# Performance work log

Hardware: AMD Instinct MI355X
Metric: run time of the kernel (lower is better)

Reference implementation:

```python
import jax, jax.numpy as jnp
import numpy as np

D_MODEL = 1024
NUM_HEADS = 16
HEAD_DIM = D_MODEL // NUM_HEADS


def setup_inputs() -> dict:
    key = jax.random.key(0)
    ks = jax.random.split(key, 12)
    B, S, D = 4, 2048, D_MODEL
    s = 1.0 / np.sqrt(D)
    return {
        "query": jax.random.normal(ks[0], (B, S, D), jnp.float32),
        "key": jax.random.normal(ks[1], (B, S, D), jnp.float32),
        "value": jax.random.normal(ks[2], (B, S, D), jnp.float32),
        "Wq": jax.random.normal(ks[3], (D, D), jnp.float32) * s,
        "bq": jax.random.normal(ks[4], (D,), jnp.float32) * 0.02,
        "Wk": jax.random.normal(ks[5], (D, D), jnp.float32) * s,
        "bk": jax.random.normal(ks[6], (D,), jnp.float32) * 0.02,
        "Wv": jax.random.normal(ks[7], (D, D), jnp.float32) * s,
        "bv": jax.random.normal(ks[8], (D,), jnp.float32) * 0.02,
        "Wo": jax.random.normal(ks[9], (D, D), jnp.float32) * s,
        "bo": jax.random.normal(ks[10], (D,), jnp.float32) * 0.02,
    }


def _split_heads(x):
    B, S, D = x.shape
    return x.reshape(B, S, NUM_HEADS, HEAD_DIM).transpose(0, 2, 1, 3)  # [B,H,S,hd]


def reference(query, key, value, Wq, bq, Wk, bk, Wv, bv, Wo, bo):
    q = _split_heads(query @ Wq + bq)
    k = _split_heads(key @ Wk + bk)
    v = _split_heads(value @ Wv + bv)
    # NOTE: original scales by 1/sqrt(d_model), not 1/sqrt(head_dim)
    scale = 1.0 / np.sqrt(D_MODEL).astype(np.float32)
    scores = jnp.einsum('bhqd,bhkd->bhqk', q, k) * scale  # [B,H,S,S]
    attn = jax.nn.softmax(scores, axis=-1)
    out = jnp.einsum('bhqk,bhkd->bhqd', attn, v)  # [B,H,S,hd]
    B, H, S, hd = out.shape
    out = out.transpose(0, 2, 1, 3).reshape(B, S, D_MODEL)
    out = out @ Wo + bo
    return out, attn
```

## Files before the change

kernel.cpp:

```cpp
#include <hip/hip_runtime.h>
#include <hip/hip_bf16.h>

typedef __bf16 bf16;
typedef __bf16 bf16x8 __attribute__((ext_vector_type(8)));
typedef __bf16 bf16x4 __attribute__((ext_vector_type(4)));
typedef float  f32x4  __attribute__((ext_vector_type(4)));

#define MFMA(A, B, C) __builtin_amdgcn_mfma_f32_16x16x32_bf16((A), (B), (C), 0, 0, 0)

static constexpr int BATCH = 4, S = 2048, D = 1024, NH = 16, HD = 64;
static constexpr int M = BATCH * S;
static constexpr float KL = 0.045084220027780106f;

__device__ __forceinline__ void gload16(const void* g, void* l) {
  __builtin_amdgcn_global_load_lds(
      (const __attribute__((address_space(1))) void*)g,
      (__attribute__((address_space(3))) void*)l, 16, 0, 0);
}

__device__ __forceinline__ float fexp2(float x) {
#if __has_builtin(__builtin_amdgcn_exp2f)
  return __builtin_amdgcn_exp2f(x);
#else
  return exp2f(x);
#endif
}

#define WAITV_BAR(n)                                        \
  asm volatile("s_waitcnt vmcnt(" #n ")" ::: "memory");     \
  __builtin_amdgcn_s_barrier();                             \
  __builtin_amdgcn_sched_barrier(0);

__global__ __launch_bounds__(256) void wt_convert(
    const float* __restrict__ W0, const float* __restrict__ W1,
    const float* __restrict__ W2, const float* __restrict__ W3,
    bf16* __restrict__ WtAll)
{
  const float* W = blockIdx.y == 0 ? W0 : blockIdx.y == 1 ? W1
                 : blockIdx.y == 2 ? W2 : W3;
  bf16* dst = WtAll + (size_t)blockIdx.y * (D * D);
  int k0 = (blockIdx.x >> 4) * 64, n0 = (blockIdx.x & 15) * 64;
  __shared__ __align__(16) bf16 T[64][72];
  int tid = threadIdx.x;
#pragma unroll
  for (int i = 0; i < 4; ++i) {
    int c = tid + i * 256, r = c >> 4, seg = c & 15;
    float4 v = *reinterpret_cast<const float4*>(W + (size_t)(k0 + r) * D + n0 + seg * 4);
    T[seg * 4 + 0][r] = (bf16)v.x; T[seg * 4 + 1][r] = (bf16)v.y;
    T[seg * 4 + 2][r] = (bf16)v.z; T[seg * 4 + 3][r] = (bf16)v.w;
  }
  __syncthreads();
#pragma unroll
  for (int i = 0; i < 2; ++i) {
    int c = tid + i * 256, r = c >> 3, seg = c & 7;
    *reinterpret_cast<bf16x8*>(dst + (size_t)(n0 + r) * D + k0 + seg * 8) =
        *reinterpret_cast<const bf16x8*>(&T[r][seg * 8]);
  }
}

__global__ __launch_bounds__(256) void x_convert(
    const float* __restrict__ X0, const float* __restrict__ X1,
    const float* __restrict__ X2, bf16* __restrict__ Y)
{
  int t = blockIdx.y;
  const float* X = t == 0 ? X0 : t == 1 ? X1 : X2;
  bf16* Yp = Y + (size_t)t * M * D;
  int idx = blockIdx.x * 256 + threadIdx.x;
#pragma unroll
  for (int i = 0; i < 4; ++i) {
    size_t j = (size_t)idx + (size_t)i * 524288;
    float4 v = reinterpret_cast<const float4*>(X)[j];
    bf16x4 o; o[0] = (bf16)v.x; o[1] = (bf16)v.y; o[2] = (bf16)v.z; o[3] = (bf16)v.w;
    reinterpret_cast<bf16x4*>(Yp)[j] = o;
  }
}

__global__ __launch_bounds__(256) void qkv_gemm(
    const bf16* __restrict__ Xb, const bf16* __restrict__ WtAll,
    const float* __restrict__ bq, const float* __restrict__ bk, const float* __restrict__ bv,
    bf16* __restrict__ Qb, bf16* __restrict__ Kb, bf16* __restrict__ Vtb)
{
  int v = blockIdx.y;
  const bf16*  X    = Xb + (size_t)v * M * D;
  const bf16*  Wt   = WtAll + (size_t)v * (D * D);
  const float* bias = v == 0 ? bq : v == 1 ? bk : bv;

  int x = blockIdx.x;
  int swz = (x & 7) * 64 + (x >> 3);
  int mt = swz >> 3, nt = swz & 7;
  int m0 = mt * 128, n0 = nt * 128;
  int tid = threadIdx.x, lane = tid & 63, w = tid >> 6;
  int wm = (w >> 1) * 64, wn = (w & 1) * 64;
  int lr = lane & 15, lg = lane >> 4;

  __shared__ __align__(16) unsigned char smem[34816];
  auto As = reinterpret_cast<bf16(*)[128][32]>(smem);
  auto Bs = reinterpret_cast<bf16(*)[128][32]>(smem + 16384);

  f32x4 acc[4][4] = {};

  int srow = w * 32 + (lane >> 2);
  int scol = (lane & 3) * 8;

  auto stage = [&](int buf, int ks) {
    const bf16* ga = X + (size_t)(m0 + srow) * D + ks * 32 + scol;
    bf16* la = &As[buf][w * 32][0];
    gload16(ga, la);
    gload16(ga + 16 * D, la + 16 * 32);
    const bf16* gb = Wt + (size_t)(n0 + srow) * D + ks * 32 + scol;
    bf16* lb = &Bs[buf][w * 32][0];
    gload16(gb, lb);
    gload16(gb + 16 * D, lb + 16 * 32);
  };

  stage(0, 0);
  for (int ks = 0; ks < 32; ++ks) {
    __syncthreads();
    if (ks < 31) stage((ks + 1) & 1, ks + 1);
    int buf = ks & 1;
    bf16x8 af[4], bfr[4];
#pragma unroll
    for (int i = 0; i < 4; ++i)
      af[i] = *reinterpret_cast<const bf16x8*>(&As[buf][wm + i * 16 + lr][8 * lg]);
#pragma unroll
    for (int j = 0; j < 4; ++j)
      bfr[j] = *reinterpret_cast<const bf16x8*>(&Bs[buf][wn + j * 16 + lr][8 * lg]);
#pragma unroll
    for (int i = 0; i < 4; ++i)
#pragma unroll
      for (int j = 0; j < 4; ++j)
        acc[i][j] = MFMA(af[i], bfr[j], acc[i][j]);
  }
  __syncthreads();

  if (v < 2) {
    bf16* Out = v == 0 ? Qb : Kb;
    float qs = v == 0 ? KL : 1.0f;
    auto Es = reinterpret_cast<bf16(*)[128]>(smem);
#pragma unroll
    for (int i = 0; i < 4; ++i)
#pragma unroll
      for (int j = 0; j < 4; ++j) {
        int n = wn + j * 16 + lr;
        float bias_n = bias[n0 + n];
#pragma unroll
        for (int r = 0; r < 4; ++r)
          Es[wm + i * 16 + 4 * lg + r][n] = (bf16)((acc[i][j][r] + bias_n) * qs);
      }
    __syncthreads();
#pragma unroll
    for (int i = 0; i < 8; ++i) {
      int c = tid + i * 256, r = c >> 4, seg = c & 15;
      int mg = m0 + r, b = mg >> 11, s = mg & 2047;
      int ng = n0 + seg * 8, h = ng >> 6, d = ng & 63;
      *reinterpret_cast<bf16x8*>(Out + (((size_t)(b * NH + h)) * S + s) * HD + d) =
          *reinterpret_cast<const bf16x8*>(&Es[r][seg * 8]);
    }
  } else {
    auto Es = reinterpret_cast<bf16(*)[136]>(smem);
#pragma unroll
    for (int i = 0; i < 4; ++i)
#pragma unroll
      for (int j = 0; j < 4; ++j) {
        int n = wn + j * 16 + lr;
        float bias_n = bias[n0 + n];
        bf16x4 t;
#pragma unroll
        for (int r = 0; r < 4; ++r) t[r] = (bf16)(acc[i][j][r] + bias_n);
        *reinterpret_cast<bf16x4*>(&Es[n][wm + i * 16 + 4 * lg]) = t;
      }
    __syncthreads();
#pragma unroll
    for (int i = 0; i < 8; ++i) {
      int c = tid + i * 256, r = c >> 4, seg = c & 15;
      int ng = n0 + r, h = ng >> 6, d = ng & 63;
      int mg = m0 + seg * 8, b = mg >> 11, s = mg & 2047;
      *reinterpret_cast<bf16x8*>(Vtb + (((size_t)(b * NH + h)) * HD + d) * S + s) =
          *reinterpret_cast<const bf16x8*>(&Es[r][seg * 8]);
    }
  }
}

__global__ __launch_bounds__(256) void attn_kernel(
    const bf16* __restrict__ Qb, const bf16* __restrict__ Kb, const bf16* __restrict__ Vtb,
    float* __restrict__ attn_out, bf16* __restrict__ ctx)
{
  int xx = blockIdx.x;
  int xcd = xx & 7, r8 = xx >> 3;
  int bh = xcd + 8 * (r8 >> 5);
  int qb = r8 & 31;
  int tid = threadIdx.x, lane = tid & 63, w = tid >> 6;
  int lr = lane & 15, lg = lane >> 4;
  int sw = lr & 7;

  __shared__ __align__(16) bf16 Ks[2][64][64];
  __shared__ __align__(16) bf16 Vs[2][64][64];
  __shared__ __align__(16) bf16 Ps[4][16][40];

  int q_row = qb * 64 + w * 16 + lr;
  const bf16x8* Qp = reinterpret_cast<const bf16x8*>(Qb + ((size_t)bh * S + q_row) * HD);
  bf16x8 qf0 = Qp[lg], qf1 = Qp[4 + lg];

  auto stageK = [&](int buf, int kc) {
    const bf16* base = Kb + ((size_t)bh * S + kc * 64) * HD;
#pragma unroll
    for (int i = 0; i < 2; ++i) {
      int c = i * 256 + tid, row = c >> 3, j = c & 7;
      gload16(base + row * HD + 8 * (j ^ (row & 7)),
              reinterpret_cast<bf16*>(&Ks[buf][0][0]) + c * 8);
    }
  };
  auto stageV = [&](int buf, int kc) {
    const bf16* base = Vtb + (size_t)bh * HD * S + kc * 64;
#pragma unroll
    for (int i = 0; i < 2; ++i) {
      int c = i * 256 + tid, row = c >> 3, j = c & 7;
      gload16(base + (size_t)row * S + 8 * (j ^ (row & 7)),
              reinterpret_cast<bf16*>(&Vs[buf][0][0]) + c * 8);
    }
  };

  float lrun = 0.f;
  stageK(0, 0);
  for (int kc = 0; kc < 32; ++kc) {
    if (kc < 31) {
      stageK((kc + 1) & 1, kc + 1);
      WAITV_BAR(2)
    } else {
      WAITV_BAR(0)
    }
    int buf = kc & 1;
#pragma unroll
    for (int sub = 0; sub < 4; ++sub) {
      int row = sub * 16 + lr;
      bf16x8 k0 = *reinterpret_cast<const bf16x8*>(&Ks[buf][row][8 * (lg ^ sw)]);
      bf16x8 k1 = *reinterpret_cast<const bf16x8*>(&Ks[buf][row][8 * ((lg + 4) ^ sw)]);
      f32x4 sa = {};
      sa = MFMA(k0, qf0, sa);
      sa = MFMA(k1, qf1, sa);
      lrun += fexp2(sa[0]) + fexp2(sa[1]) + fexp2(sa[2]) + fexp2(sa[3]);
    }
    __builtin_amdgcn_s_barrier();
  }
  lrun += __shfl_xor(lrun, 16);
  lrun += __shfl_xor(lrun, 32);
  float lg2l = __log2f(lrun);

  f32x4 oacc[4] = {};
  float* arow = attn_out + ((size_t)bh * S + q_row) * S;

  auto computeB = [&](int buf, int kc) {
#pragma unroll
    for (int half = 0; half < 2; ++half) {
      f32x4 sg[2];
#pragma unroll
      for (int t = 0; t < 2; ++t) {
        int row = (half * 2 + t) * 16 + lr;
        bf16x8 k0 = *reinterpret_cast<const bf16x8*>(&Ks[buf][row][8 * (lg ^ sw)]);
        bf16x8 k1 = *reinterpret_cast<const bf16x8*>(&Ks[buf][row][8 * ((lg + 4) ^ sw)]);
        f32x4 sa = {};
        sa = MFMA(k0, qf0, sa);
        sa = MFMA(k1, qf1, sa);
        sg[t] = sa;
      }
#pragma unroll
      for (int t = 0; t < 2; ++t) {
        f32x4 pv;
        bf16x4 pb;
#pragma unroll
        for (int r = 0; r < 4; ++r) {
          float p = fexp2(sg[t][r] - lg2l);
          pv[r] = p; pb[r] = (bf16)p;
        }
        __builtin_nontemporal_store(pv,
            reinterpret_cast<f32x4*>(arow + kc * 64 + half * 32 + t * 16 + 4 * lg));
        *reinterpret_cast<bf16x4*>(&Ps[w][lr][t * 16 + 4 * lg]) = pb;
      }
      bf16x8 pa = *reinterpret_cast<const bf16x8*>(&Ps[w][lr][8 * lg]);
#pragma unroll
      for (int dt = 0; dt < 4; ++dt) {
        int vrow = dt * 16 + lr;
        bf16x8 vb = *reinterpret_cast<const bf16x8*>(&Vs[buf][vrow][8 * ((half * 4 + lg) ^ sw)]);
        oacc[dt] = MFMA(pa, vb, oacc[dt]);
      }
    }
  };

  stageK(0, 0); stageV(0, 0);
  stageK(1, 1); stageV(1, 1);
  WAITV_BAR(4)
  computeB(0, 0);
  __builtin_amdgcn_s_barrier();

  for (int kc = 1; kc < 32; ++kc) {
    if (kc < 31) {
      stageK((kc + 1) & 1, kc + 1);
      stageV((kc + 1) & 1, kc + 1);
      WAITV_BAR(8)
    } else {
      WAITV_BAR(4)
    }
    computeB(kc & 1, kc);
    __builtin_amdgcn_s_barrier();
  }

  int b = bh >> 4, h = bh & 15;
  bf16* cs = reinterpret_cast<bf16*>(&Ks[0][0][0]) + w * (16 * 72);
#pragma unroll
  for (int dt = 0; dt < 4; ++dt)
#pragma unroll
    for (int r = 0; r < 4; ++r)
      cs[(4 * lg + r) * 72 + dt * 16 + lr] = (bf16)oacc[dt][r];
  asm volatile("s_waitcnt lgkmcnt(0)" ::: "memory");
  __builtin_amdgcn_sched_barrier(0);
  {
    int r_ = lane >> 2, cb = (lane & 3) * 16;
    int qr = qb * 64 + w * 16 + r_;
    bf16* cp = ctx + ((size_t)b * S + qr) * D + h * HD + cb;
    *reinterpret_cast<bf16x8*>(cp)     = *reinterpret_cast<const bf16x8*>(&cs[r_ * 72 + cb]);
    *reinterpret_cast<bf16x8*>(cp + 8) = *reinterpret_cast<const bf16x8*>(&cs[r_ * 72 + cb + 8]);
  }
}

__global__ __launch_bounds__(256) void out_gemm(
    const bf16* __restrict__ ctx, const bf16* __restrict__ Wto,
    const float* __restrict__ bo, float* __restrict__ Out)
{
  int x = blockIdx.x;
  int swz = (x & 7) * 64 + (x >> 3);
  int mt = swz >> 3, nt = swz & 7;
  int m0 = mt * 128, n0 = nt * 128;
  int tid = threadIdx.x, lane = tid & 63, w = tid >> 6;
  int wm = (w >> 1) * 64, wn = (w & 1) * 64;
  int lr = lane & 15, lg = lane >> 4;

  __shared__ __align__(16) bf16 As[2][128][32];
  __shared__ __align__(16) bf16 Bs[2][128][32];

  f32x4 acc[4][4] = {};

  int srow = w * 32 + (lane >> 2);
  int scol = (lane & 3) * 8;

  auto stage = [&](int buf, int ks) {
    const bf16* ga = ctx + (size_t)(m0 + srow) * D + ks * 32 + scol;
    bf16* la = &As[buf][w * 32][0];
    gload16(ga, la);
    gload16(ga + 16 * D, la + 16 * 32);
    const bf16* gb = Wto + (size_t)(n0 + srow) * D + ks * 32 + scol;
    bf16* lb = &Bs[buf][w * 32][0];
    gload16(gb, lb);
    gload16(gb + 16 * D, lb + 16 * 32);
  };

  stage(0, 0);
  for (int ks = 0; ks < 32; ++ks) {
    __syncthreads();
    if (ks < 31) stage((ks + 1) & 1, ks + 1);
    int buf = ks & 1;
    bf16x8 af[4], bfr[4];
#pragma unroll
    for (int i = 0; i < 4; ++i)
      af[i] = *reinterpret_cast<const bf16x8*>(&As[buf][wm + i * 16 + lr][8 * lg]);
#pragma unroll
    for (int j = 0; j < 4; ++j)
      bfr[j] = *reinterpret_cast<const bf16x8*>(&Bs[buf][wn + j * 16 + lr][8 * lg]);
#pragma unroll
    for (int i = 0; i < 4; ++i)
#pragma unroll
      for (int j = 0; j < 4; ++j)
        acc[i][j] = MFMA(af[i], bfr[j], acc[i][j]);
  }

#pragma unroll
  for (int i = 0; i < 4; ++i)
#pragma unroll
    for (int j = 0; j < 4; ++j) {
      int n = n0 + wn + j * 16 + lr;
      float bias_n = bo[n];
#pragma unroll
      for (int r = 0; r < 4; ++r)
        Out[(size_t)(m0 + wm + i * 16 + 4 * lg + r) * D + n] = acc[i][j][r] + bias_n;
    }
}

extern "C" void kernel_launch(void* const* d_in, const int* in_sizes, int n_in,
                              void* d_out, int out_size, void* d_ws, size_t ws_size,
                              hipStream_t stream)
{
  const float* query = (const float*)d_in[0];
  const float* key   = (const float*)d_in[1];
  const float* value = (const float*)d_in[2];
  const float* Wq = (const float*)d_in[3]; const float* bq = (const float*)d_in[4];
  const float* Wk = (const float*)d_in[5]; const float* bk = (const float*)d_in[6];
  const float* Wv = (const float*)d_in[7]; const float* bv = (const float*)d_in[8];
  const float* Wo = (const float*)d_in[9]; const float* bo = (const float*)d_in[10];

  float* out  = (float*)d_out;
  float* attn = out + (size_t)M * D;

  char* ws = (char*)d_ws;
  const size_t MiB = 1048576;
  bf16* WtAll = (bf16*)ws;
  bf16* Xb    = (bf16*)(ws + 8 * MiB);
  bf16* Qb    = (bf16*)(ws + 56 * MiB);
  bf16* Kb    = (bf16*)(ws + 72 * MiB);
  bf16* Vtb   = (bf16*)(ws + 88 * MiB);
  bf16* ctx   = Xb;

  wt_convert<<<dim3(256, 4), 256, 0, stream>>>(Wq, Wk, Wv, Wo, WtAll);
  x_convert<<<dim3(2048, 3), 256, 0, stream>>>(query, key, value, Xb);
  qkv_gemm<<<dim3(512, 3), 256, 0, stream>>>(Xb, WtAll, bq, bk, bv, Qb, Kb, Vtb);
  attn_kernel<<<dim3(2048), 256, 0, stream>>>(Qb, Kb, Vtb, attn, ctx);
  out_gemm<<<dim3(512), 256, 0, stream>>>(ctx, WtAll + (size_t)3 * D * D, bo, out);
}
```

Baseline: 456.1 us.

## Switch attention kernel to 32x32 MFMA with 2x2 query/key wave split

```diff
diff --git a/kernel.cpp b/kernel.cpp
--- a/kernel.cpp
+++ b/kernel.cpp
@@ -4,9 +4,13 @@
 typedef __bf16 bf16;
 typedef __bf16 bf16x8 __attribute__((ext_vector_type(8)));
 typedef __bf16 bf16x4 __attribute__((ext_vector_type(4)));
+typedef __bf16 bf16x2 __attribute__((ext_vector_type(2)));
 typedef float  f32x4  __attribute__((ext_vector_type(4)));
-
-#define MFMA(A, B, C) __builtin_amdgcn_mfma_f32_16x16x32_bf16((A), (B), (C), 0, 0, 0)
+typedef float  f32x16 __attribute__((ext_vector_type(16)));
+typedef unsigned int u32;
+
+#define MFMA(A, B, C)   __builtin_amdgcn_mfma_f32_16x16x32_bf16((A), (B), (C), 0, 0, 0)
+#define MFMA32(A, B, C) __builtin_amdgcn_mfma_f32_32x32x16_bf16((A), (B), (C), 0, 0, 0)
 
 static constexpr int BATCH = 4, S = 2048, D = 1024, NH = 16, HD = 64;
 static constexpr int M = BATCH * S;
@@ -25,6 +29,14 @@
   return exp2f(x);
 #endif
 }
+
+__device__ __forceinline__ u32 pack2(float a, float b) {
+  union { bf16x2 h; u32 u; } c;
+  c.h = (bf16x2){(bf16)a, (bf16)b};
+  return c.u;
+}
+
+union U4 { u32 w[4]; bf16x8 v; };
 
 #define WAITV_BAR(n)                                        \
   asm volatile("s_waitcnt vmcnt(" #n ")" ::: "memory");     \
@@ -190,16 +202,19 @@
   int bh = xcd + 8 * (r8 >> 5);
   int qb = r8 & 31;
   int tid = threadIdx.x, lane = tid & 63, w = tid >> 6;
-  int lr = lane & 15, lg = lane >> 4;
-  int sw = lr & 7;
+  int q32 = lane & 31, hi = lane >> 5;
+  int qh = w & 1, kh = w >> 1;
 
   __shared__ __align__(16) bf16 Ks[2][64][64];
   __shared__ __align__(16) bf16 Vs[2][64][64];
-  __shared__ __align__(16) bf16 Ps[4][16][40];
-
-  int q_row = qb * 64 + w * 16 + lr;
-  const bf16x8* Qp = reinterpret_cast<const bf16x8*>(Qb + ((size_t)bh * S + q_row) * HD);
-  bf16x8 qf0 = Qp[lg], qf1 = Qp[4 + lg];
+  __shared__ float sums[2][64];
+
+  int q_row = qb * 64 + qh * 32 + q32;
+  const bf16* Qrow = Qb + ((size_t)bh * S + q_row) * HD;
+  bf16x8 qreg[4];
+#pragma unroll
+  for (int c = 0; c < 4; ++c)
+    qreg[c] = *reinterpret_cast<const bf16x8*>(Qrow + c * 16 + 8 * hi);
 
   auto stageK = [&](int buf, int kc) {
     const bf16* base = Kb + ((size_t)bh * S + kc * 64) * HD;
@@ -219,6 +234,8 @@
               reinterpret_cast<bf16*>(&Vs[buf][0][0]) + c * 8);
     }
   };
+
+  int krow = kh * 32 + q32, ks7 = krow & 7;
 
   float lrun = 0.f;
   stageK(0, 0);
@@ -230,58 +247,66 @@
       WAITV_BAR(0)
     }
     int buf = kc & 1;
-#pragma unroll
-    for (int sub = 0; sub < 4; ++sub) {
-      int row = sub * 16 + lr;
-      bf16x8 k0 = *reinterpret_cast<const bf16x8*>(&Ks[buf][row][8 * (lg ^ sw)]);
-      bf16x8 k1 = *reinterpret_cast<const bf16x8*>(&Ks[buf][row][8 * ((lg + 4) ^ sw)]);
-      f32x4 sa = {};
-      sa = MFMA(k0, qf0, sa);
-      sa = MFMA(k1, qf1, sa);
-      lrun += fexp2(sa[0]) + fexp2(sa[1]) + fexp2(sa[2]) + fexp2(sa[3]);
-    }
+    f32x16 sa = {};
+#pragma unroll
+    for (int c = 0; c < 4; ++c) {
+      bf16x8 kf = *reinterpret_cast<const bf16x8*>(&Ks[buf][krow][8 * ((2 * c + hi) ^ ks7)]);
+      sa = MFMA32(kf, qreg[c], sa);
+    }
+#pragma unroll
+    for (int r = 0; r < 16; ++r) lrun += fexp2(sa[r]);
     __builtin_amdgcn_s_barrier();
   }
-  lrun += __shfl_xor(lrun, 16);
   lrun += __shfl_xor(lrun, 32);
-  float lg2l = __log2f(lrun);
-
-  f32x4 oacc[4] = {};
+  if (hi == 0) sums[kh][qh * 32 + q32] = lrun;
+  __syncthreads();
+  float lg2l = __log2f(sums[0][qh * 32 + q32] + sums[1][qh * 32 + q32]);
+
+  f32x16 oaccA = {}, oaccB = {};
   float* arow = attn_out + ((size_t)bh * S + q_row) * S;
 
   auto computeB = [&](int buf, int kc) {
-#pragma unroll
-    for (int half = 0; half < 2; ++half) {
-      f32x4 sg[2];
-#pragma unroll
-      for (int t = 0; t < 2; ++t) {
-        int row = (half * 2 + t) * 16 + lr;
-        bf16x8 k0 = *reinterpret_cast<const bf16x8*>(&Ks[buf][row][8 * (lg ^ sw)]);
-        bf16x8 k1 = *reinterpret_cast<const bf16x8*>(&Ks[buf][row][8 * ((lg + 4) ^ sw)]);
-        f32x4 sa = {};
-        sa = MFMA(k0, qf0, sa);
-        sa = MFMA(k1, qf1, sa);
-        sg[t] = sa;
+    f32x16 sa = {};
+#pragma unroll
+    for (int c = 0; c < 4; ++c) {
+      bf16x8 kf = *reinterpret_cast<const bf16x8*>(&Ks[buf][krow][8 * ((2 * c + hi) ^ ks7)]);
+      sa = MFMA32(kf, qreg[c], sa);
+    }
+    u32 pku[8];
+#pragma unroll
+    for (int rq = 0; rq < 4; ++rq) {
+      f32x4 pv;
+#pragma unroll
+      for (int j = 0; j < 4; ++j) pv[j] = fexp2(sa[rq * 4 + j] - lg2l);
+      __builtin_nontemporal_store(pv,
+          reinterpret_cast<f32x4*>(arow + kc * 64 + kh * 32 + 8 * rq + 4 * hi));
+      pku[rq * 2 + 0] = pack2(pv[0], pv[1]);
+      pku[rq * 2 + 1] = pack2(pv[2], pv[3]);
+    }
+#pragma unroll
+    for (int c2 = 0; c2 < 2; ++c2) {
+      u32 myw0 = hi ? pku[4 * c2 + 2] : pku[4 * c2 + 0];
+      u32 myw1 = hi ? pku[4 * c2 + 3] : pku[4 * c2 + 1];
+      u32 sdw0 = hi ? pku[4 * c2 + 0] : pku[4 * c2 + 2];
+      u32 sdw1 = hi ? pku[4 * c2 + 1] : pku[4 * c2 + 3];
+      u32 r0 = __shfl_xor(sdw0, 32);
+      u32 r1 = __shfl_xor(sdw1, 32);
+      U4 f;
+      f.w[0] = hi ? r0 : myw0;
+      f.w[1] = hi ? r1 : myw1;
+      f.w[2] = hi ? myw0 : r0;
+      f.w[3] = hi ? myw1 : r1;
+      {
+        int vrow = q32, vs7 = vrow & 7;
+        bf16x8 vf = *reinterpret_cast<const bf16x8*>(
+            &Vs[buf][vrow][8 * ((4 * kh + 2 * c2 + hi) ^ vs7)]);
+        oaccA = MFMA32(f.v, vf, oaccA);
       }
-#pragma unroll
-      for (int t = 0; t < 2; ++t) {
-        f32x4 pv;
-        bf16x4 pb;
-#pragma unroll
-        for (int r = 0; r < 4; ++r) {
-          float p = fexp2(sg[t][r] - lg2l);
-          pv[r] = p; pb[r] = (bf16)p;
-        }
-        __builtin_nontemporal_store(pv,
-            reinterpret_cast<f32x4*>(arow + kc * 64 + half * 32 + t * 16 + 4 * lg));
-        *reinterpret_cast<bf16x4*>(&Ps[w][lr][t * 16 + 4 * lg]) = pb;
-      }
-      bf16x8 pa = *reinterpret_cast<const bf16x8*>(&Ps[w][lr][8 * lg]);
-#pragma unroll
-      for (int dt = 0; dt < 4; ++dt) {
-        int vrow = dt * 16 + lr;
-        bf16x8 vb = *reinterpret_cast<const bf16x8*>(&Vs[buf][vrow][8 * ((half * 4 + lg) ^ sw)]);
-        oacc[dt] = MFMA(pa, vb, oacc[dt]);
+      {
+        int vrow = 32 + q32, vs7 = vrow & 7;
+        bf16x8 vf = *reinterpret_cast<const bf16x8*>(
+            &Vs[buf][vrow][8 * ((4 * kh + 2 * c2 + hi) ^ vs7)]);
+        oaccB = MFMA32(f.v, vf, oaccB);
       }
     }
   };
@@ -304,21 +329,36 @@
     __builtin_amdgcn_s_barrier();
   }
 
-  int b = bh >> 4, h = bh & 15;
-  bf16* cs = reinterpret_cast<bf16*>(&Ks[0][0][0]) + w * (16 * 72);
-#pragma unroll
-  for (int dt = 0; dt < 4; ++dt)
-#pragma unroll
-    for (int r = 0; r < 4; ++r)
-      cs[(4 * lg + r) * 72 + dt * 16 + lr] = (bf16)oacc[dt][r];
-  asm volatile("s_waitcnt lgkmcnt(0)" ::: "memory");
-  __builtin_amdgcn_sched_barrier(0);
+  float* fbuf = reinterpret_cast<float*>(&Ks[0][0][0]);
+  if (kh == 1) {
+#pragma unroll
+    for (int reg = 0; reg < 16; ++reg) {
+      int qloc = (reg & 3) + 8 * (reg >> 2) + 4 * hi;
+      fbuf[(qh * 32 + qloc) * 64 + q32]      = oaccA[reg];
+      fbuf[(qh * 32 + qloc) * 64 + 32 + q32] = oaccB[reg];
+    }
+  }
+  __syncthreads();
+  bf16* cs = reinterpret_cast<bf16*>(&Vs[0][0][0]);
+  if (kh == 0) {
+#pragma unroll
+    for (int reg = 0; reg < 16; ++reg) {
+      int qloc = (reg & 3) + 8 * (reg >> 2) + 4 * hi;
+      cs[(qh * 32 + qloc) * 72 + q32] =
+          (bf16)(oaccA[reg] + fbuf[(qh * 32 + qloc) * 64 + q32]);
+      cs[(qh * 32 + qloc) * 72 + 32 + q32] =
+          (bf16)(oaccB[reg] + fbuf[(qh * 32 + qloc) * 64 + 32 + q32]);
+    }
+  }
+  __syncthreads();
   {
-    int r_ = lane >> 2, cb = (lane & 3) * 16;
-    int qr = qb * 64 + w * 16 + r_;
-    bf16* cp = ctx + ((size_t)b * S + qr) * D + h * HD + cb;
-    *reinterpret_cast<bf16x8*>(cp)     = *reinterpret_cast<const bf16x8*>(&cs[r_ * 72 + cb]);
-    *reinterpret_cast<bf16x8*>(cp + 8) = *reinterpret_cast<const bf16x8*>(&cs[r_ * 72 + cb + 8]);
+    int b = bh >> 4, h = bh & 15;
+    int row = tid >> 2, cseg = (tid & 3) * 16;
+    bf16* cp = ctx + ((size_t)b * S + qb * 64 + row) * D + h * HD + cseg;
+    *reinterpret_cast<bf16x8*>(cp) =
+        *reinterpret_cast<const bf16x8*>(&cs[row * 72 + cseg]);
+    *reinterpret_cast<bf16x8*>(cp + 8) =
+        *reinterpret_cast<const bf16x8*>(&cs[row * 72 + cseg + 8]);
   }
 }
 
```

After: 1.266 ms. 178% more time.
